# Performance work log

Hardware: AMD Instinct MI355X
Metric: run time of the kernel (lower is better)

The kernel has to match this reference:

```python
import jax, jax.numpy as jnp
import numpy as np

EPS = 1e-6

def setup_inputs() -> dict:
    key = jax.random.key(0)
    k1, k2, k3, k4, k5 = jax.random.split(key, 5)
    M, K, N = 8192, 4096, 4096  # K == N required by the original's shape usage
    x = jax.random.normal(k1, (M, K), dtype=jnp.float32)
    W1 = jax.random.normal(k2, (K, N), dtype=jnp.float32)
    W2 = jax.random.normal(k3, (N, K), dtype=jnp.float32)
    D = jax.random.normal(k4, (M, K), dtype=jnp.float32)   # epilogue bias/residual operand
    g = jax.random.normal(k5, (K,), dtype=jnp.float32)     # rmsnorm weight
    return {"x": x, "W1": W1, "W2": W2, "D": D, "g": g}

def _rmsnorm(h, g):
    # normalize over the last dim, then scale by learned weight g
    rms = jax.lax.rsqrt(jnp.mean(h * h, axis=-1, keepdims=True) + EPS)
    return h * rms * g

def reference(x, W1, W2, D, g):
    # mm1: fp8 GEMM with epilogue add of D  ->  [M, N]
    h = jnp.einsum('mk,kn->mn', x, W1) + D
    # fused RMSNorm epilogue
    h = _rmsnorm(h, g)
    # mm2: fp8 GEMM with epilogue add of D  ->  [M, K]
    out = jnp.einsum('mn,nk->mk', h, W2) + D
    return out
```

## Files before the change

kernel.cpp:

```cpp
#include <hip/hip_runtime.h>
#include <hip/hip_bf16.h>

typedef float f32x4 __attribute__((ext_vector_type(4)));
typedef short short8 __attribute__((ext_vector_type(8)));
typedef unsigned short ushort8 __attribute__((ext_vector_type(8)));
typedef unsigned short ushort4v __attribute__((ext_vector_type(4)));

static __device__ __forceinline__ unsigned short f2bf(float f) {
  unsigned u = __builtin_bit_cast(unsigned, f);
  u += 0x7fffu + ((u >> 16) & 1u);
  return (unsigned short)(u >> 16);
}
static __device__ __forceinline__ float bf2f(unsigned short s) {
  return __builtin_bit_cast(float, (unsigned)s << 16);
}

__global__ __launch_bounds__(256) void k_cvt_bf16(const float* __restrict__ in,
                                                  unsigned short* __restrict__ out,
                                                  int n8) {
  int i = blockIdx.x * 256 + threadIdx.x;
  if (i >= n8) return;
  const float4* p = (const float4*)in + (size_t)i * 2;
  float4 a = p[0], b = p[1];
  ushort8 o;
  o[0] = f2bf(a.x); o[1] = f2bf(a.y); o[2] = f2bf(a.z); o[3] = f2bf(a.w);
  o[4] = f2bf(b.x); o[5] = f2bf(b.y); o[6] = f2bf(b.z); o[7] = f2bf(b.w);
  *(ushort8*)(out + (size_t)i * 8) = o;
}

__global__ __launch_bounds__(256) void k_transpose_cvt(const float* __restrict__ in,
                                                       unsigned short* __restrict__ out,
                                                       int R, int C) {
  __shared__ float tile[64][65];
  int c0 = blockIdx.x * 64;
  int r0 = blockIdx.y * 64;
  int t = threadIdx.x;
  int tr = t >> 4;
  int tc = (t & 15) << 2;
  for (int i = 0; i < 4; ++i) {
    int r = tr + (i << 4);
    float4 v = *(const float4*)&in[(size_t)(r0 + r) * C + c0 + tc];
    tile[r][tc] = v.x; tile[r][tc + 1] = v.y; tile[r][tc + 2] = v.z; tile[r][tc + 3] = v.w;
  }
  __syncthreads();
  for (int i = 0; i < 4; ++i) {
    int c = tr + (i << 4);
    ushort4v o;
    o[0] = f2bf(tile[tc + 0][c]);
    o[1] = f2bf(tile[tc + 1][c]);
    o[2] = f2bf(tile[tc + 2][c]);
    o[3] = f2bf(tile[tc + 3][c]);
    *(ushort4v*)&out[(size_t)(c0 + c) * R + r0 + tc] = o;
  }
}

template <int OUT_BF16>
__global__ __launch_bounds__(256) void k_gemm(const unsigned short* __restrict__ A,
                                              const unsigned short* __restrict__ Bt,
                                              const float* __restrict__ D,
                                              void* __restrict__ out,
                                              int M, int N, int K) {
  constexpr int BM = 128, BN = 128, BK = 32;
  __shared__ unsigned short As[BM * BK];
  __shared__ unsigned short Bs[BN * BK];

  int nwg = gridDim.x;
  int bid = blockIdx.x;
  int cpx = nwg >> 3;
  int swz = (bid & 7) * cpx + (bid >> 3);
  int nbn = N / BN;
  int bm0 = (swz / nbn) * BM;
  int bn0 = (swz % nbn) * BN;

  int t = threadIdx.x;
  int lane = t & 63;
  int w = t >> 6;
  int wm = (w >> 1) << 6;
  int wn = (w & 1) << 6;

  const unsigned short* gA = A + (size_t)(bm0 + (t >> 2)) * K + ((t & 3) << 3);
  const unsigned short* gB = Bt + (size_t)(bn0 + (t >> 2)) * K + ((t & 3) << 3);
  unsigned short* ldsA = As + t * 8;
  unsigned short* ldsB = Bs + t * 8;

  f32x4 acc[4][4];
  for (int i = 0; i < 4; ++i)
    for (int j = 0; j < 4; ++j)
      acc[i][j] = f32x4{0.f, 0.f, 0.f, 0.f};

  int row = lane & 15;
  int ks = (lane >> 4) << 3;
  const int nk = K >> 5;

  for (int kt = 0; kt < nk; ++kt) {
    __builtin_amdgcn_global_load_lds((const __attribute__((address_space(1))) void*)gA,
                                     (__attribute__((address_space(3))) void*)ldsA, 16, 0, 0);
    __builtin_amdgcn_global_load_lds((const __attribute__((address_space(1))) void*)(gA + (size_t)64 * K),
                                     (__attribute__((address_space(3))) void*)(ldsA + 2048), 16, 0, 0);
    __builtin_amdgcn_global_load_lds((const __attribute__((address_space(1))) void*)gB,
                                     (__attribute__((address_space(3))) void*)ldsB, 16, 0, 0);
    __builtin_amdgcn_global_load_lds((const __attribute__((address_space(1))) void*)(gB + (size_t)64 * K),
                                     (__attribute__((address_space(3))) void*)(ldsB + 2048), 16, 0, 0);
    gA += BK;
    gB += BK;
    __syncthreads();

    short8 af[4], bfr[4];
    for (int i = 0; i < 4; ++i)
      af[i] = *(const short8*)&As[(wm + (i << 4) + row) * BK + ks];
    for (int j = 0; j < 4; ++j)
      bfr[j] = *(const short8*)&Bs[(wn + (j << 4) + row) * BK + ks];
    for (int i = 0; i < 4; ++i)
      for (int j = 0; j < 4; ++j)
        acc[i][j] = __builtin_amdgcn_mfma_f32_16x16x32_bf16(af[i], bfr[j], acc[i][j], 0, 0, 0);
    __syncthreads();
  }

  int r0 = bm0 + wm + ((lane >> 4) << 2);
  int cc = bn0 + wn + (lane & 15);
  for (int i = 0; i < 4; ++i) {
    for (int j = 0; j < 4; ++j) {
      int rbase = r0 + (i << 4);
      int c = cc + (j << 4);
      for (int rr = 0; rr < 4; ++rr) {
        size_t idx = (size_t)(rbase + rr) * N + c;
        float v = acc[i][j][rr] + D[idx];
        if (OUT_BF16)
          ((unsigned short*)out)[idx] = f2bf(v);
        else
          ((float*)out)[idx] = v;
      }
    }
  }
}

__global__ __launch_bounds__(256) void k_rmsnorm(unsigned short* __restrict__ h,
                                                 const float* __restrict__ g,
                                                 int N) {
  __shared__ float red[4];
  int rowi = blockIdx.x;
  unsigned short* p = h + (size_t)rowi * N;
  int t = threadIdx.x;
  int base = t << 4;
  ushort8 v0 = *(const ushort8*)&p[base];
  ushort8 v1 = *(const ushort8*)&p[base + 8];
  float f[16];
  float ss = 0.f;
  for (int j = 0; j < 8; ++j) { f[j] = bf2f(v0[j]); ss += f[j] * f[j]; }
  for (int j = 0; j < 8; ++j) { f[8 + j] = bf2f(v1[j]); ss += f[8 + j] * f[8 + j]; }
  for (int off = 32; off > 0; off >>= 1) ss += __shfl_xor(ss, off);
  if ((t & 63) == 0) red[t >> 6] = ss;
  __syncthreads();
  float total = red[0] + red[1] + red[2] + red[3];
  float scale = rsqrtf(total / (float)N + 1e-6f);
  float4 g0 = *(const float4*)&g[base];
  float4 g1 = *(const float4*)&g[base + 4];
  float4 g2 = *(const float4*)&g[base + 8];
  float4 g3 = *(const float4*)&g[base + 12];
  ushort8 o0, o1;
  o0[0] = f2bf(f[0] * scale * g0.x);  o0[1] = f2bf(f[1] * scale * g0.y);
  o0[2] = f2bf(f[2] * scale * g0.z);  o0[3] = f2bf(f[3] * scale * g0.w);
  o0[4] = f2bf(f[4] * scale * g1.x);  o0[5] = f2bf(f[5] * scale * g1.y);
  o0[6] = f2bf(f[6] * scale * g1.z);  o0[7] = f2bf(f[7] * scale * g1.w);
  o1[0] = f2bf(f[8] * scale * g2.x);  o1[1] = f2bf(f[9] * scale * g2.y);
  o1[2] = f2bf(f[10] * scale * g2.z); o1[3] = f2bf(f[11] * scale * g2.w);
  o1[4] = f2bf(f[12] * scale * g3.x); o1[5] = f2bf(f[13] * scale * g3.y);
  o1[6] = f2bf(f[14] * scale * g3.z); o1[7] = f2bf(f[15] * scale * g3.w);
  *(ushort8*)&p[base] = o0;
  *(ushort8*)&p[base + 8] = o1;
}

extern "C" void kernel_launch(void* const* d_in, const int* in_sizes, int n_in,
                              void* d_out, int out_size, void* d_ws, size_t ws_size,
                              hipStream_t stream) {
  const float* x  = (const float*)d_in[0];
  const float* W1 = (const float*)d_in[1];
  const float* W2 = (const float*)d_in[2];
  const float* D  = (const float*)d_in[3];
  const float* g  = (const float*)d_in[4];
  const int M = 8192, K = 4096, N = 4096;

  char* ws = (char*)d_ws;
  unsigned short* xb  = (unsigned short*)ws;
  unsigned short* w1t = (unsigned short*)(ws + (size_t)M * K * 2);
  unsigned short* w2t = (unsigned short*)(ws + (size_t)M * K * 2 + (size_t)K * N * 2);
  unsigned short* h   = (unsigned short*)(ws + (size_t)M * K * 2 + (size_t)2 * K * N * 2);

  int n8 = (M * K) / 8;
  k_cvt_bf16<<<n8 / 256, 256, 0, stream>>>(x, xb, n8);
  k_transpose_cvt<<<dim3(N / 64, K / 64), 256, 0, stream>>>(W1, w1t, K, N);
  k_transpose_cvt<<<dim3(K / 64, N / 64), 256, 0, stream>>>(W2, w2t, N, K);
  k_gemm<1><<<(M / 128) * (N / 128), 256, 0, stream>>>(xb, w1t, D, (void*)h, M, N, K);
  k_rmsnorm<<<M, 256, 0, stream>>>(h, g, N);
  k_gemm<0><<<(M / 128) * (K / 128), 256, 0, stream>>>(h, w2t, D, d_out, M, K, N);
}
```

Baseline: 1.313 ms.

## Rewrite GEMM as 256x256 tile, 8-wave, double-buffered LDS pipeline

Replaces the 128x128, BK=32, single-buffer GEMM with a 256x256 tile, 512-thread kernel using BK=64, XOR-swizzled LDS and a double-buffered global_load_lds prefetch. The MFMA work is split into quarter stages interleaved with LDS reads and async loads, using explicit barriers, waitcnts and s_setprio. This targets the stall-heavy load/sync/compute loop and raises data reuse per tile. The cost is much higher register and LDS pressure (128KB LDS, 32 accumulators) and fragile hand-placed waitcnt ordering.

```diff
diff --git a/kernel.cpp b/kernel.cpp
--- a/kernel.cpp
+++ b/kernel.cpp
@@ -54,76 +54,165 @@
   }
 }
 
+
+#define LDSW(off) ({ int _o = (off); _o ^= ((_o >> 9) & 1) << 5; \
+                     *(const short8*)((const char*)lds + _o); })
+
+#define RD_A(cur, half) do { \
+  _Pragma("unroll") for (int i_ = 0; i_ < 4; ++i_) { \
+    _Pragma("unroll") for (int ks_ = 0; ks_ < 2; ++ks_) \
+      a[i_][ks_] = LDSW((cur) + abase + ((half) * 64 + i_ * 16) * 128 + ks_ * 64); } \
+} while (0)
+
+#define RD_B(cur, j0) do { \
+  _Pragma("unroll") for (int j_ = 0; j_ < 2; ++j_) { \
+    _Pragma("unroll") for (int ks_ = 0; ks_ < 2; ++ks_) \
+      b[(j0) + j_][ks_] = LDSW((cur) + bbase + ((j0) + j_) * 2048 + ks_ * 64); } \
+} while (0)
+
+#define MMQ(i0, j0) do { \
+  _Pragma("unroll") for (int di_ = 0; di_ < 4; ++di_) { \
+    _Pragma("unroll") for (int dj_ = 0; dj_ < 2; ++dj_) { \
+      _Pragma("unroll") for (int ks_ = 0; ks_ < 2; ++ks_) \
+        acc[(i0) + di_][(j0) + dj_] = __builtin_amdgcn_mfma_f32_16x16x32_bf16( \
+            a[di_][ks_], b[(j0) + dj_][ks_], acc[(i0) + di_][(j0) + dj_], 0, 0, 0); } } \
+} while (0)
+
+#define STG(ptr, T, base, h) do { \
+  __builtin_amdgcn_global_load_lds( \
+      (const __attribute__((address_space(1))) void*)((ptr) + (size_t)(T) * 64 + soff[2 * (h)]), \
+      (__attribute__((address_space(3))) void*)((char*)lds + (base) + reld[2 * (h)]), 16, 0, 0); \
+  __builtin_amdgcn_global_load_lds( \
+      (const __attribute__((address_space(1))) void*)((ptr) + (size_t)(T) * 64 + soff[2 * (h) + 1]), \
+      (__attribute__((address_space(3))) void*)((char*)lds + (base) + reld[2 * (h) + 1]), 16, 0, 0); \
+} while (0)
+
+#define PBAR() __builtin_amdgcn_s_barrier()
+#define LGKM0() asm volatile("s_waitcnt lgkmcnt(0)" ::: "memory")
+#define VMW4() asm volatile("s_waitcnt vmcnt(4)" ::: "memory")
+#define VMW0() asm volatile("s_waitcnt vmcnt(0)" ::: "memory")
+
 template <int OUT_BF16>
-__global__ __launch_bounds__(256) void k_gemm(const unsigned short* __restrict__ A,
-                                              const unsigned short* __restrict__ Bt,
-                                              const float* __restrict__ D,
-                                              void* __restrict__ out,
-                                              int M, int N, int K) {
-  constexpr int BM = 128, BN = 128, BK = 32;
-  __shared__ unsigned short As[BM * BK];
-  __shared__ unsigned short Bs[BN * BK];
+__global__ __launch_bounds__(512, 2) void k_gemm256(const unsigned short* __restrict__ A,
+                                                    const unsigned short* __restrict__ Bt,
+                                                    const float* __restrict__ D,
+                                                    void* __restrict__ out,
+                                                    int M, int N, int K) {
+  __shared__ unsigned short lds[65536];
 
   int nwg = gridDim.x;
   int bid = blockIdx.x;
   int cpx = nwg >> 3;
   int swz = (bid & 7) * cpx + (bid >> 3);
-  int nbn = N / BN;
-  int bm0 = (swz / nbn) * BM;
-  int bn0 = (swz % nbn) * BN;
-
-  int t = threadIdx.x;
-  int lane = t & 63;
-  int w = t >> 6;
-  int wm = (w >> 1) << 6;
-  int wn = (w & 1) << 6;
-
-  const unsigned short* gA = A + (size_t)(bm0 + (t >> 2)) * K + ((t & 3) << 3);
-  const unsigned short* gB = Bt + (size_t)(bn0 + (t >> 2)) * K + ((t & 3) << 3);
-  unsigned short* ldsA = As + t * 8;
-  unsigned short* ldsB = Bs + t * 8;
-
-  f32x4 acc[4][4];
-  for (int i = 0; i < 4; ++i)
+  int nbn = N >> 8;
+  int bm0 = (swz / nbn) << 8;
+  int bn0 = (swz % nbn) << 8;
+
+  int tid = threadIdx.x;
+  int lane = tid & 63;
+  int w = tid >> 6;
+  int wr = w >> 2, wc = w & 3;
+
+  const unsigned short* pA = A + (size_t)bm0 * K;
+  const unsigned short* pB = Bt + (size_t)bn0 * K;
+
+  size_t soff[4];
+  int reld[4];
+#pragma unroll
+  for (int c = 0; c < 4; ++c) {
+    int rel = ((c >> 1) << 14) + ((c & 1) << 13) + tid * 16;
+    int u = rel ^ (((rel >> 9) & 1) << 5);
+    soff[c] = (size_t)(u >> 7) * K + ((u & 127) >> 1);
+    reld[c] = rel;
+  }
+
+  int laneRow = lane & 15;
+  int laneKb = (lane >> 4) << 4;
+  int abase = (wr * 128 + laneRow) * 128 + laneKb;
+  int bbase = 32768 + (wc * 64 + laneRow) * 128 + laneKb;
+
+  f32x4 acc[8][4];
+#pragma unroll
+  for (int i = 0; i < 8; ++i)
+#pragma unroll
     for (int j = 0; j < 4; ++j)
       acc[i][j] = f32x4{0.f, 0.f, 0.f, 0.f};
 
-  int row = lane & 15;
-  int ks = (lane >> 4) << 3;
-  const int nk = K >> 5;
-
-  for (int kt = 0; kt < nk; ++kt) {
-    __builtin_amdgcn_global_load_lds((const __attribute__((address_space(1))) void*)gA,
-                                     (__attribute__((address_space(3))) void*)ldsA, 16, 0, 0);
-    __builtin_amdgcn_global_load_lds((const __attribute__((address_space(1))) void*)(gA + (size_t)64 * K),
-                                     (__attribute__((address_space(3))) void*)(ldsA + 2048), 16, 0, 0);
-    __builtin_amdgcn_global_load_lds((const __attribute__((address_space(1))) void*)gB,
-                                     (__attribute__((address_space(3))) void*)ldsB, 16, 0, 0);
-    __builtin_amdgcn_global_load_lds((const __attribute__((address_space(1))) void*)(gB + (size_t)64 * K),
-                                     (__attribute__((address_space(3))) void*)(ldsB + 2048), 16, 0, 0);
-    gA += BK;
-    gB += BK;
-    __syncthreads();
-
-    short8 af[4], bfr[4];
-    for (int i = 0; i < 4; ++i)
-      af[i] = *(const short8*)&As[(wm + (i << 4) + row) * BK + ks];
-    for (int j = 0; j < 4; ++j)
-      bfr[j] = *(const short8*)&Bs[(wn + (j << 4) + row) * BK + ks];
-    for (int i = 0; i < 4; ++i)
-      for (int j = 0; j < 4; ++j)
-        acc[i][j] = __builtin_amdgcn_mfma_f32_16x16x32_bf16(af[i], bfr[j], acc[i][j], 0, 0, 0);
-    __syncthreads();
-  }
-
-  int r0 = bm0 + wm + ((lane >> 4) << 2);
-  int cc = bn0 + wn + (lane & 15);
-  for (int i = 0; i < 4; ++i) {
+  short8 a[4][2], b[4][2];
+
+  const int NT = K >> 6;
+
+  STG(pB, 0, 32768, 0); STG(pB, 0, 32768, 1);
+  STG(pA, 0, 0, 0);     STG(pA, 0, 0, 1);
+  STG(pB, 1, 98304, 0); STG(pB, 1, 98304, 1);
+  VMW4();
+  PBAR();
+
+  int T = 0;
+  for (; T < NT - 2; T += 2) {
+    RD_A(0, 0); RD_B(0, 0);
+    STG(pA, T + 1, 65536, 0);
+    PBAR(); LGKM0(); __builtin_amdgcn_s_setprio(1); MMQ(0, 0); __builtin_amdgcn_s_setprio(0); PBAR();
+
+    RD_B(0, 2);
+    STG(pA, T + 1, 65536, 1);
+    PBAR(); LGKM0(); __builtin_amdgcn_s_setprio(1); MMQ(0, 2); __builtin_amdgcn_s_setprio(0); PBAR();
+
+    RD_A(0, 1);
+    STG(pB, T + 2, 32768, 0);
+    PBAR(); LGKM0(); __builtin_amdgcn_s_setprio(1); MMQ(4, 2); __builtin_amdgcn_s_setprio(0); PBAR();
+
+    STG(pB, T + 2, 32768, 1);
+    VMW4();
+    PBAR(); __builtin_amdgcn_s_setprio(1); MMQ(4, 0); __builtin_amdgcn_s_setprio(0); PBAR();
+
+    RD_A(65536, 0); RD_B(65536, 0);
+    STG(pA, T + 2, 0, 0);
+    PBAR(); LGKM0(); __builtin_amdgcn_s_setprio(1); MMQ(0, 0); __builtin_amdgcn_s_setprio(0); PBAR();
+
+    RD_B(65536, 2);
+    STG(pA, T + 2, 0, 1);
+    PBAR(); LGKM0(); __builtin_amdgcn_s_setprio(1); MMQ(0, 2); __builtin_amdgcn_s_setprio(0); PBAR();
+
+    RD_A(65536, 1);
+    STG(pB, T + 3, 98304, 0);
+    PBAR(); LGKM0(); __builtin_amdgcn_s_setprio(1); MMQ(4, 2); __builtin_amdgcn_s_setprio(0); PBAR();
+
+    STG(pB, T + 3, 98304, 1);
+    VMW4();
+    PBAR(); __builtin_amdgcn_s_setprio(1); MMQ(4, 0); __builtin_amdgcn_s_setprio(0); PBAR();
+  }
+
+  RD_A(0, 0); RD_B(0, 0);
+  STG(pA, T + 1, 65536, 0);
+  PBAR(); LGKM0(); __builtin_amdgcn_s_setprio(1); MMQ(0, 0); __builtin_amdgcn_s_setprio(0); PBAR();
+  RD_B(0, 2);
+  STG(pA, T + 1, 65536, 1);
+  PBAR(); LGKM0(); __builtin_amdgcn_s_setprio(1); MMQ(0, 2); __builtin_amdgcn_s_setprio(0); PBAR();
+  RD_A(0, 1);
+  PBAR(); LGKM0(); __builtin_amdgcn_s_setprio(1); MMQ(4, 2); __builtin_amdgcn_s_setprio(0); PBAR();
+  VMW0();
+  PBAR(); __builtin_amdgcn_s_setprio(1); MMQ(4, 0); __builtin_amdgcn_s_setprio(0); PBAR();
+
+  RD_A(65536, 0); RD_B(65536, 0);
+  PBAR(); LGKM0(); __builtin_amdgcn_s_setprio(1); MMQ(0, 0); __builtin_amdgcn_s_setprio(0); PBAR();
+  RD_B(65536, 2);
+  PBAR(); LGKM0(); __builtin_amdgcn_s_setprio(1); MMQ(0, 2); __builtin_amdgcn_s_setprio(0); PBAR();
+  RD_A(65536, 1);
+  PBAR(); LGKM0(); __builtin_amdgcn_s_setprio(1); MMQ(4, 2); __builtin_amdgcn_s_setprio(0); PBAR();
+  MMQ(4, 0);
+
+  int er = bm0 + wr * 128 + ((lane >> 4) << 2);
+  int ec = bn0 + wc * 64 + laneRow;
+#pragma unroll
+  for (int i = 0; i < 8; ++i) {
+#pragma unroll
     for (int j = 0; j < 4; ++j) {
-      int rbase = r0 + (i << 4);
-      int c = cc + (j << 4);
+      int r = er + i * 16;
+      int c = ec + j * 16;
+#pragma unroll
       for (int rr = 0; rr < 4; ++rr) {
-        size_t idx = (size_t)(rbase + rr) * N + c;
+        size_t idx = (size_t)(r + rr) * N + c;
         float v = acc[i][j][rr] + D[idx];
         if (OUT_BF16)
           ((unsigned short*)out)[idx] = f2bf(v);
@@ -190,7 +279,7 @@
   k_cvt_bf16<<<n8 / 256, 256, 0, stream>>>(x, xb, n8);
   k_transpose_cvt<<<dim3(N / 64, K / 64), 256, 0, stream>>>(W1, w1t, K, N);
   k_transpose_cvt<<<dim3(K / 64, N / 64), 256, 0, stream>>>(W2, w2t, N, K);
-  k_gemm<1><<<(M / 128) * (N / 128), 256, 0, stream>>>(xb, w1t, D, (void*)h, M, N, K);
+  k_gemm256<1><<<(M / 256) * (N / 256), 512, 0, stream>>>(xb, w1t, D, (void*)h, M, N, K);
   k_rmsnorm<<<M, 256, 0, stream>>>(h, g, N);
-  k_gemm<0><<<(M / 128) * (K / 128), 256, 0, stream>>>(h, w2t, D, d_out, M, K, N);
-}
+  k_gemm256<0><<<(M / 256) * (K / 256), 512, 0, stream>>>(h, w2t, D, d_out, M, K, N);
+}
```

After: 1.295 ms. No clear change (-1.4%).
